# Kernel tuning notes

Measured on AMD Instinct MI355X. Metric: run time of the kernel, lower is better.

The kernel has to match this reference:

```python
import jax, jax.numpy as jnp
import numpy as np

B, N, D, H = 4, 2048, 1024, 16
DH = D // H

def setup_inputs() -> dict:
    key = jax.random.key(0)
    kx, kqkv, ko = jax.random.split(key, 3)
    x = jax.random.normal(kx, (B, N, D), dtype=jnp.float32)
    # torch Linear weights: [out, in]; scale like default init
    W_qkv = jax.random.normal(kqkv, (3 * D, D), dtype=jnp.float32) * (1.0 / np.sqrt(D))
    W_out = jax.random.normal(ko, (D, D), dtype=jnp.float32) * (1.0 / np.sqrt(D))
    return {"x": x, "W_qkv": W_qkv, "W_out": W_out}

def reference(x, W_qkv, W_out):
    Bk, Nk, C = x.shape
    qkv = jnp.einsum('bnc,oc->bno', x, W_qkv)  # [B,N,3D]
    qkv = qkv.reshape(Bk, Nk, 3, H, DH).transpose(2, 0, 3, 1, 4)  # [3,B,H,N,DH]
    q, k, v = qkv[0], qkv[1], qkv[2]
    att = jnp.einsum('bhnd,bhmd->bhnm', q, k) * (1.0 / np.sqrt(DH))
    mask = jnp.triu(jnp.ones((Nk, Nk), dtype=bool), k=1)  # True above diagonal
    att = jnp.where(mask, -jnp.inf, att)
    att = jax.nn.softmax(att, axis=-1)
    y = jnp.einsum('bhnm,bhmd->bhnd', att, v)  # [B,H,N,DH]
    y = y.transpose(0, 2, 1, 3).reshape(Bk, Nk, C)
    return jnp.einsum('bnc,oc->bno', y, W_out)
```

## Files before the change

### kernel.cpp

```cpp
#include <hip/hip_runtime.h>
#include <hip/hip_bf16.h>
#include <stdint.h>

#define Bb 4
#define Nn 2048
#define Dd 1024
#define Hh 16
#define DHd 64
#define Mm (Bb*Nn)
#define D3 (3*Dd)

typedef unsigned short u16;
typedef unsigned int u32;
typedef __attribute__((ext_vector_type(8))) short bf16x8;
typedef __attribute__((ext_vector_type(4))) float f32x4;
typedef __attribute__((ext_vector_type(2))) unsigned int u32x2;
typedef __attribute__((ext_vector_type(4))) unsigned int u32x4;

__device__ __forceinline__ u16 f2bf(float f) {
    unsigned int u = __float_as_uint(f);
    u = (u + 0x7FFFu + ((u >> 16) & 1u)) >> 16;
    return (u16)u;
}

__device__ __forceinline__ u32 cvtpk_bf16(float lo, float hi) {
    u32 r;
    asm("v_cvt_pk_bf16_f32 %0, %1, %2" : "=v"(r) : "v"(lo), "v"(hi));
    return r;
}

__device__ __forceinline__ float fexp2(float x) {
    float r;
    asm("v_exp_f32 %0, %1" : "=v"(r) : "v"(x));
    return r;
}

#define GLOAD16(g, l)                                                          \
    __builtin_amdgcn_global_load_lds(                                          \
        (const __attribute__((address_space(1))) unsigned int*)(g),            \
        (__attribute__((address_space(3))) unsigned int*)(l), 16, 0, 0)

__global__ void cvt_f32_bf16(const float* __restrict__ in, u16* __restrict__ out, int n4) {
    int i = blockIdx.x * blockDim.x + threadIdx.x;
    int stride = gridDim.x * blockDim.x;
    for (; i < n4; i += stride) {
        float4 v = ((const float4*)in)[i];
        u16 o0 = f2bf(v.x), o1 = f2bf(v.y), o2 = f2bf(v.z), o3 = f2bf(v.w);
        unsigned int lo = (unsigned int)o0 | ((unsigned int)o1 << 16);
        unsigned int hi = (unsigned int)o2 | ((unsigned int)o3 << 16);
        ((uint2*)out)[i] = make_uint2(lo, hi);
    }
}

__global__ void cvt_f32_bf16_s(const float* __restrict__ in, u16* __restrict__ out,
                               int n4, int cut4, float s) {
    int i = blockIdx.x * blockDim.x + threadIdx.x;
    int stride = gridDim.x * blockDim.x;
    for (; i < n4; i += stride) {
        float4 v = ((const float4*)in)[i];
        float sc = (i < cut4) ? s : 1.0f;
        u16 o0 = f2bf(v.x * sc), o1 = f2bf(v.y * sc), o2 = f2bf(v.z * sc), o3 = f2bf(v.w * sc);
        unsigned int lo = (unsigned int)o0 | ((unsigned int)o1 << 16);
        unsigned int hi = (unsigned int)o2 | ((unsigned int)o3 << 16);
        ((uint2*)out)[i] = make_uint2(lo, hi);
    }
}

template<int OUT_F32>
__global__ __launch_bounds__(256) void gemm_bt(const u16* __restrict__ A,
                                               const u16* __restrict__ Bm,
                                               void* __restrict__ C,
                                               int M, int Nout, int K) {
    __shared__ u16 As[128 * 64];
    __shared__ u16 Bs[128 * 64];
    const int t = threadIdx.x;
    const int lane = t & 63;
    const int w = t >> 6;
    const int wr = w >> 1, wc = w & 1;
    const int l15 = lane & 15, l4 = lane >> 4;
    const int m0 = blockIdx.y * 128;
    const int n0 = blockIdx.x * 128;

    f32x4 acc[4][4] = {};

    for (int k0 = 0; k0 < K; k0 += 64) {
        __syncthreads();
#pragma unroll
        for (int i = 0; i < 4; i++) {
            int chunk = i * 256 + t;
            int row = chunk >> 3;
            int csw = ((chunk & 7) ^ (row & 7)) << 3;
            GLOAD16(A + (size_t)(m0 + row) * K + k0 + csw, &As[chunk * 8]);
            GLOAD16(Bm + (size_t)(n0 + row) * K + k0 + csw, &Bs[chunk * 8]);
        }
        __syncthreads();

#pragma unroll
        for (int kh = 0; kh < 2; kh++) {
            bf16x8 a[4], b[4];
#pragma unroll
            for (int mi = 0; mi < 4; mi++) {
                int row = wr * 64 + mi * 16 + l15;
                a[mi] = *(const bf16x8*)&As[row * 64 + (((kh * 4 + l4) ^ (row & 7)) << 3)];
            }
#pragma unroll
            for (int nj = 0; nj < 4; nj++) {
                int row = wc * 64 + nj * 16 + l15;
                b[nj] = *(const bf16x8*)&Bs[row * 64 + (((kh * 4 + l4) ^ (row & 7)) << 3)];
            }
#pragma unroll
            for (int mi = 0; mi < 4; mi++)
#pragma unroll
                for (int nj = 0; nj < 4; nj++)
                    acc[mi][nj] = __builtin_amdgcn_mfma_f32_16x16x32_bf16(a[mi], b[nj], acc[mi][nj], 0, 0, 0);
        }
    }

#pragma unroll
    for (int mi = 0; mi < 4; mi++) {
#pragma unroll
        for (int nj = 0; nj < 4; nj++) {
            int col = n0 + wc * 64 + nj * 16 + l15;
#pragma unroll
            for (int r = 0; r < 4; r++) {
                int row = m0 + wr * 64 + mi * 16 + l4 * 4 + r;
                float v = acc[mi][nj][r];
                if (OUT_F32)
                    ((float*)C)[(size_t)row * Nout + col] = v;
                else
                    ((u16*)C)[(size_t)row * Nout + col] = f2bf(v);
            }
        }
    }
}

__global__ __launch_bounds__(512) void attn(const u16* __restrict__ qkv, u16* __restrict__ y) {
    __shared__ u16 Kt[2][64 * 64];
    __shared__ u16 Vt[2][64 * 64];

    const int t = threadIdx.x;
    const int lane = t & 63;
    const int w = t >> 6;
    const int l15 = lane & 15, l4 = lane >> 4;
    const int bh = blockIdx.x * 8 + (blockIdx.y & 7);
    const int pairidx = blockIdx.y >> 3;
    const int b = bh >> 4, h = bh & 15;

    const u16* qbase = qkv + (size_t)(b * Nn) * D3 + h * DHd;
    const u16* Kg = qbase + Dd;
    const u16* Vg = qbase + 2 * Dd;

    const int krow = t >> 3;
    const int ksw = (((t & 7) ^ (krow & 7)) << 3);
    const int vi = t & 31;
    const int vsd = (t >> 5) * 4;
    const int vchunk = (2 * vi) >> 3;
    const int vcol = (2 * vi) & 7;

    const bool hi2 = (lane >> 5) & 1;
    const bool bit0 = (lane >> 4) & 1;
    const int sgrp = lane & 48;

    bool mgt[4];
#pragma unroll
    for (int r = 0; r < 4; r++) mgt[r] = (l4 * 4 + r) > l15;

    for (int pass = 0; pass < 2; ++pass) {
        const int qt = pass == 0 ? pairidx : (15 - pairidx);
        const int q0 = qt * 128;
        const int ktmax = 2 * qt + 1;
        const int qwmin = q0 + w * 16;

        bf16x8 qf[2];
        {
            const u16* qrow = qbase + (size_t)(qwmin + l15) * D3;
            qf[0] = *(const bf16x8*)(qrow + l4 * 8);
            qf[1] = *(const bf16x8*)(qrow + 32 + l4 * 8);
        }

        f32x4 o[4] = {};
        float m_ = -1e30f;
        float l_ = 0.f;

        u32x2 va, vb_;

        GLOAD16(Kg + (size_t)krow * D3 + ksw, &Kt[0][t * 8]);
        {
            const u16* vr = Vg + (size_t)(2 * vi) * D3 + vsd;
            va = *(const u32x2*)vr;
            vb_ = *(const u32x2*)(vr + D3);
        }
        asm volatile("s_waitcnt vmcnt(0)" ::: "memory");
        {
            u16 av[4], bv[4];
            *(u32x2*)av = va; *(u32x2*)bv = vb_;
#pragma unroll
            for (int j = 0; j < 4; j++) {
                int d = vsd + j;
                u32 word = (u32)av[j] | ((u32)bv[j] << 16);
                *(u32*)&Vt[0][d * 64 + ((vchunk ^ (d & 7)) << 3) + vcol] = word;
            }
        }
        __syncthreads();

        int cur = 0;
        for (int kt = 0; kt <= ktmax; ++kt) {
            const int k0 = kt * 64;
            const int havenext = (kt < ktmax);

            if (havenext) {
                const int nk0 = k0 + 64;
                GLOAD16(Kg + (size_t)(nk0 + krow) * D3 + ksw, &Kt[cur ^ 1][t * 8]);
                const u16* vr = Vg + (size_t)(nk0 + 2 * vi) * D3 + vsd;
                va = *(const u32x2*)vr;
                vb_ = *(const u32x2*)(vr + D3);
            }

            const int dks = (qwmin - k0) >> 4;

            if (dks >= 0) {
                const int kcm = dks < 3 ? dks : 3;
                const int kgm = (dks >> 1) < 1 ? (dks >> 1) : 1;

                f32x4 sv[4];
                float vmax = -3.0e38f;
                __builtin_amdgcn_s_setprio(1);
#pragma unroll
                for (int kc = 0; kc < 4; ++kc) {
                    if (kc <= kcm) {
                        f32x4 s = {};
                        int row = kc * 16 + l15;
                        int sw = row & 7;
                        bf16x8 kf0 = *(const bf16x8*)&Kt[cur][row * 64 + ((l4 ^ sw) << 3)];
                        bf16x8 kf1 = *(const bf16x8*)&Kt[cur][row * 64 + (((4 + l4) ^ sw) << 3)];
                        s = __builtin_amdgcn_mfma_f32_16x16x32_bf16(kf0, qf[0], s, 0, 0, 0);
                        s = __builtin_amdgcn_mfma_f32_16x16x32_bf16(kf1, qf[1], s, 0, 0, 0);
                        const bool bmask = (kc == dks);
#pragma unroll
                        for (int r = 0; r < 4; r++) {
                            float x = s[r];
                            if (bmask && mgt[r]) x = -1e30f;
                            sv[kc][r] = x;
                            vmax = fmaxf(vmax, x);
                        }
                    }
                }
                __builtin_amdgcn_s_setprio(0);

                vmax = fmaxf(vmax, __shfl_xor(vmax, 16));
                vmax = fmaxf(vmax, __shfl_xor(vmax, 32));

                if (!__all(vmax <= m_ + 8.f)) {
                    float newm = fmaxf(m_, vmax);
                    float corr = fexp2(m_ - newm);
                    l_ *= corr;
                    float corr_o[4];
#pragma unroll
                    for (int r = 0; r < 4; ++r)
                        corr_o[r] = __shfl(corr, sgrp | (((lane >> 4) & 3) * 4 + r));
#pragma unroll
                    for (int db = 0; db < 4; db++)
#pragma unroll
                        for (int r = 0; r < 4; r++) o[db][r] *= corr_o[r];
                    m_ = newm;
                }

                u32 up[4][2];
#pragma unroll
                for (int kc = 0; kc < 4; ++kc) {
                    if (kc <= kcm) {
                        float p0 = fexp2(sv[kc][0] - m_);
                        float p1 = fexp2(sv[kc][1] - m_);
                        float p2 = fexp2(sv[kc][2] - m_);
                        float p3 = fexp2(sv[kc][3] - m_);
                        l_ += (p0 + p1) + (p2 + p3);
                        up[kc][0] = cvtpk_bf16(p0, p1);
                        up[kc][1] = cvtpk_bf16(p2, p3);
                    } else {
                        up[kc][0] = 0u;
                        up[kc][1] = 0u;
                    }
                }

                __builtin_amdgcn_s_setprio(1);
#pragma unroll
                for (int kg = 0; kg < 2; kg++) {
                    if (kg <= kgm) {
                        u32 paya0 = hi2 ? up[2 * kg + 1][0] : up[2 * kg][0];
                        u32 paya1 = hi2 ? up[2 * kg + 1][1] : up[2 * kg][1];
                        u32 payb0 = hi2 ? up[2 * kg][0] : up[2 * kg + 1][0];
                        u32 payb1 = hi2 ? up[2 * kg][1] : up[2 * kg + 1][1];
                        u32 a16_0 = (u32)__shfl_xor((int)paya0, 16);
                        u32 a16_1 = (u32)__shfl_xor((int)paya1, 16);
                        u32 a32_0 = (u32)__shfl_xor((int)payb0, 32);
                        u32 a32_1 = (u32)__shfl_xor((int)payb1, 32);
                        u32 a48_0 = (u32)__shfl_xor((int)payb0, 48);
                        u32 a48_1 = (u32)__shfl_xor((int)payb1, 48);
                        u32x4 tt;
                        tt[0] = hi2 ? (bit0 ? a16_0 : a32_0) : (bit0 ? a48_0 : paya0);
                        tt[1] = hi2 ? (bit0 ? a16_1 : a32_1) : (bit0 ? a48_1 : paya1);
                        tt[2] = hi2 ? (bit0 ? paya0 : a48_0) : (bit0 ? a32_0 : a16_0);
                        tt[3] = hi2 ? (bit0 ? paya1 : a48_1) : (bit0 ? a32_1 : a16_1);
                        union { u32x4 u; bf16x8 b; } pa;
                        pa.u = tt;
#pragma unroll
                        for (int db = 0; db < 4; db++) {
                            int d = db * 16 + l15;
                            bf16x8 vb = *(const bf16x8*)&Vt[cur][d * 64 + (((kg * 4 + l4) ^ (d & 7)) << 3)];
                            o[db] = __builtin_amdgcn_mfma_f32_16x16x32_bf16(pa.b, vb, o[db], 0, 0, 0);
                        }
                    }
                }
                __builtin_amdgcn_s_setprio(0);
            }

            if (havenext) {
                asm volatile("s_waitcnt vmcnt(0)" ::: "memory");
                u16 av[4], bv[4];
                *(u32x2*)av = va; *(u32x2*)bv = vb_;
#pragma unroll
                for (int j = 0; j < 4; j++) {
                    int d = vsd + j;
                    u32 word = (u32)av[j] | ((u32)bv[j] << 16);
                    *(u32*)&Vt[cur ^ 1][d * 64 + ((vchunk ^ (d & 7)) << 3) + vcol] = word;
                }
            }
            __syncthreads();
            cur ^= 1;
        }

        l_ += __shfl_xor(l_, 16);
        l_ += __shfl_xor(l_, 32);
        float linv = 1.f / l_;
        float linv_o[4];
#pragma unroll
        for (int r = 0; r < 4; ++r)
            linv_o[r] = __shfl(linv, sgrp | (((lane >> 4) & 3) * 4 + r));
#pragma unroll
        for (int r = 0; r < 4; r++) {
            int qg = qwmin + l4 * 4 + r;
            u16* yrow = y + (size_t)(b * Nn + qg) * Dd + h * DHd;
#pragma unroll
            for (int db = 0; db < 4; db++)
                yrow[db * 16 + l15] = f2bf(o[db][r] * linv_o[r]);
        }
    }
}

extern "C" void kernel_launch(void* const* d_in, const int* in_sizes, int n_in,
                              void* d_out, int out_size, void* d_ws, size_t ws_size,
                              hipStream_t stream) {
    const float* x = (const float*)d_in[0];
    const float* Wqkv = (const float*)d_in[1];
    const float* Wout = (const float*)d_in[2];

    char* ws = (char*)d_ws;
    size_t off = 0;
    u16* xb = (u16*)(ws + off);    off += (size_t)Mm * Dd * 2;
    u16* wqkvb = (u16*)(ws + off); off += (size_t)D3 * Dd * 2;
    u16* woutb = (u16*)(ws + off); off += (size_t)Dd * Dd * 2;
    u16* qkv = (u16*)(ws + off);   off += (size_t)Mm * D3 * 2;
    u16* yb = (u16*)(ws + off);    off += (size_t)Mm * Dd * 2;

    const float SCL = 0.125f * 1.4426950408889634f;

    cvt_f32_bf16<<<4096, 256, 0, stream>>>(x, xb, Mm * Dd / 4);
    cvt_f32_bf16_s<<<1024, 256, 0, stream>>>(Wqkv, wqkvb, D3 * Dd / 4, Dd * Dd / 4, SCL);
    cvt_f32_bf16<<<512, 256, 0, stream>>>(Wout, woutb, Dd * Dd / 4);

    gemm_bt<0><<<dim3(D3 / 128, Mm / 128), 256, 0, stream>>>(xb, wqkvb, qkv, Mm, D3, Dd);
    attn<<<dim3(Nn / 256, Bb * Hh), 512, 0, stream>>>(qkv, yb);
    gemm_bt<1><<<dim3(Dd / 128, Mm / 128), 256, 0, stream>>>(yb, woutb, d_out, Mm, Dd, Dd);
}
```

Baseline: 178.4 us.

## Fuse conversion kernels, remap GEMM tiles across XCDs, skip wave max shuffles

```diff
diff --git a/kernel.cpp b/kernel.cpp
--- a/kernel.cpp
+++ b/kernel.cpp
@@ -40,29 +40,24 @@
         (const __attribute__((address_space(1))) unsigned int*)(g),            \
         (__attribute__((address_space(3))) unsigned int*)(l), 16, 0, 0)
 
-__global__ void cvt_f32_bf16(const float* __restrict__ in, u16* __restrict__ out, int n4) {
+__global__ void cvt_all(const float* __restrict__ x, const float* __restrict__ wqkv,
+                        const float* __restrict__ wout, u16* __restrict__ xb,
+                        u16* __restrict__ wqkvb, u16* __restrict__ woutb, float s) {
+    const int A4 = Mm * Dd / 4;
+    const int B4 = D3 * Dd / 4;
+    const int C4 = Dd * Dd / 4;
+    const int QCUT = Dd * Dd / 4;
+    const int total = A4 + B4 + C4;
     int i = blockIdx.x * blockDim.x + threadIdx.x;
-    int stride = gridDim.x * blockDim.x;
-    for (; i < n4; i += stride) {
-        float4 v = ((const float4*)in)[i];
-        u16 o0 = f2bf(v.x), o1 = f2bf(v.y), o2 = f2bf(v.z), o3 = f2bf(v.w);
-        unsigned int lo = (unsigned int)o0 | ((unsigned int)o1 << 16);
-        unsigned int hi = (unsigned int)o2 | ((unsigned int)o3 << 16);
-        ((uint2*)out)[i] = make_uint2(lo, hi);
-    }
-}
-
-__global__ void cvt_f32_bf16_s(const float* __restrict__ in, u16* __restrict__ out,
-                               int n4, int cut4, float s) {
-    int i = blockIdx.x * blockDim.x + threadIdx.x;
-    int stride = gridDim.x * blockDim.x;
-    for (; i < n4; i += stride) {
-        float4 v = ((const float4*)in)[i];
-        float sc = (i < cut4) ? s : 1.0f;
+    const int stride = gridDim.x * blockDim.x;
+    for (; i < total; i += stride) {
+        const float* src; u16* dst; int j; float sc = 1.f;
+        if (i < A4) { src = x; dst = xb; j = i; }
+        else if (i < A4 + B4) { j = i - A4; src = wqkv; dst = wqkvb; if (j < QCUT) sc = s; }
+        else { j = i - A4 - B4; src = wout; dst = woutb; }
+        float4 v = ((const float4*)src)[j];
         u16 o0 = f2bf(v.x * sc), o1 = f2bf(v.y * sc), o2 = f2bf(v.z * sc), o3 = f2bf(v.w * sc);
-        unsigned int lo = (unsigned int)o0 | ((unsigned int)o1 << 16);
-        unsigned int hi = (unsigned int)o2 | ((unsigned int)o3 << 16);
-        ((uint2*)out)[i] = make_uint2(lo, hi);
+        ((uint2*)dst)[j] = make_uint2((u32)o0 | ((u32)o1 << 16), (u32)o2 | ((u32)o3 << 16));
     }
 }
 
@@ -78,8 +73,13 @@
     const int w = t >> 6;
     const int wr = w >> 1, wc = w & 1;
     const int l15 = lane & 15, l4 = lane >> 4;
-    const int m0 = blockIdx.y * 128;
-    const int n0 = blockIdx.x * 128;
+
+    const int gx = gridDim.x;
+    const int linear = blockIdx.y * gx + blockIdx.x;
+    const int cpx = (gx * gridDim.y) >> 3;
+    const int tile = (linear & 7) * cpx + (linear >> 3);
+    const int m0 = (tile / gx) * 128;
+    const int n0 = (tile % gx) * 128;
 
     f32x4 acc[4][4] = {};
 
@@ -223,7 +223,7 @@
                 const int kgm = (dks >> 1) < 1 ? (dks >> 1) : 1;
 
                 f32x4 sv[4];
-                float vmax = -3.0e38f;
+                float lm = -3.0e38f;
                 __builtin_amdgcn_s_setprio(1);
 #pragma unroll
                 for (int kc = 0; kc < 4; ++kc) {
@@ -241,16 +241,15 @@
                             float x = s[r];
                             if (bmask && mgt[r]) x = -1e30f;
                             sv[kc][r] = x;
-                            vmax = fmaxf(vmax, x);
+                            lm = fmaxf(lm, x);
                         }
                     }
                 }
                 __builtin_amdgcn_s_setprio(0);
 
-                vmax = fmaxf(vmax, __shfl_xor(vmax, 16));
-                vmax = fmaxf(vmax, __shfl_xor(vmax, 32));
-
-                if (!__all(vmax <= m_ + 8.f)) {
+                if (!__all(lm <= m_ + 8.f)) {
+                    float vmax = fmaxf(lm, __shfl_xor(lm, 16));
+                    vmax = fmaxf(vmax, __shfl_xor(vmax, 32));
                     float newm = fmaxf(m_, vmax);
                     float corr = fexp2(m_ - newm);
                     l_ *= corr;
@@ -364,11 +363,9 @@
 
     const float SCL = 0.125f * 1.4426950408889634f;
 
-    cvt_f32_bf16<<<4096, 256, 0, stream>>>(x, xb, Mm * Dd / 4);
-    cvt_f32_bf16_s<<<1024, 256, 0, stream>>>(Wqkv, wqkvb, D3 * Dd / 4, Dd * Dd / 4, SCL);
-    cvt_f32_bf16<<<512, 256, 0, stream>>>(Wout, woutb, Dd * Dd / 4);
+    cvt_all<<<4096, 256, 0, stream>>>(x, Wqkv, Wout, xb, wqkvb, woutb, SCL);
 
     gemm_bt<0><<<dim3(D3 / 128, Mm / 128), 256, 0, stream>>>(xb, wqkvb, qkv, Mm, D3, Dd);
-    attn<<<dim3(Nn / 256, Bb * Hh), 512, 0, stream>>>(qkv, yb);
+    attn<<<dim3(8, 64), 512, 0, stream>>>(qkv, yb);
     gemm_bt<1><<<dim3(Dd / 128, Mm / 128), 256, 0, stream>>>(yb, woutb, d_out, Mm, Dd, Dd);
 }
```

After: 172.9 us. 1.03x faster.
